# Kernel tuning notes

Measured on AMD Instinct MI355X. Metric: run time of the kernel, lower is better.

Reference implementation:

```python
import jax, jax.numpy as jnp
from jax import lax
import numpy as np

B, N, E, F = 32, 256, 8, 16
NEIGH = 31            # neighbourhood_size
K1 = NEIGH + 1        # subgraph size = neigh_size + 1


def setup_inputs() -> dict:
    rng = np.random.default_rng(0)
    # Connected symmetric adjacency: backbone chain + random extra pairs (no self loops).
    A = np.zeros((B, N, N), np.float32)
    i = np.arange(N - 1)
    A[:, i, i + 1] = 1.0
    A[:, i + 1, i] = 1.0
    for b in range(B):
        pairs = rng.integers(0, N, size=(N, 2))
        pairs = pairs[pairs[:, 0] != pairs[:, 1]]
        A[b, pairs[:, 0], pairs[:, 1]] = 1.0
        A[b, pairs[:, 1], pairs[:, 0]] = 1.0
    A[:, np.arange(N), np.arange(N)] = 0.0
    key = jax.random.key(0)
    k1, k2 = jax.random.split(key)
    edges = jax.random.normal(k1, (B, N, N, E), dtype=jnp.float32)
    feats = jax.random.normal(k2, (B, N, F), dtype=jnp.float32)
    return {"adj_batch": jnp.asarray(A), "edges_batch": edges, "features_batch": feats}


def _bfs(adj_bool, start):
    """Ordered BFS from `start`, collecting K1 vertices (matches get_neighbours:
    FIFO queue, neighbours enqueued in ascending index order, dedup vs seen)."""
    n = adj_bool.shape[0]
    queue = jnp.zeros((n + 1,), jnp.int32).at[0].set(start)  # slot n is a dummy sink
    seen = jnp.zeros((n,), bool).at[start].set(True)
    processed = jnp.zeros((K1,), jnp.int32)

    def body(i, st):
        queue, seen, head, tail, processed = st
        cur = queue[head]
        processed = processed.at[i].set(cur)
        nbr = adj_bool[cur] & ~seen                      # new frontier, index order
        cum = jnp.cumsum(nbr.astype(jnp.int32))
        pos = jnp.where(nbr, tail + cum - 1, n)          # compacted queue slots
        queue = queue.at[pos].set(jnp.arange(n, dtype=jnp.int32))
        return queue, seen | nbr, head + 1, tail + cum[-1], processed

    st = lax.fori_loop(0, K1, body, (queue, seen, jnp.int32(0), jnp.int32(1), processed))
    return st[4]  # [K1] BFS ordering


def reference(adj_batch, edges_batch, features_batch):
    adj_bool = adj_batch != 0
    starts = jnp.arange(adj_batch.shape[1], dtype=jnp.int32)
    # proc: [B, N, K1] local->original vertex mapping per (graph, centre vertex)
    proc = jax.vmap(lambda ab: jax.vmap(lambda s: _bfs(ab, s))(starts))(adj_bool)

    def gather(adj, edges, feats, p):
        pi = p[:, :, None]                               # [N, K1, 1]
        pj = p[:, None, :]                               # [N, 1, K1]
        sub_adj = adj[pi, pj]                            # [N, K1, K1]
        mask = (sub_adj != 0)[..., None]
        sub_edges = jnp.where(mask, edges[pi, pj], 0.0)  # [N, K1, K1, E]
        sub_feats = feats[p]                             # [N, K1, F]
        return sub_adj, sub_edges, sub_feats

    return jax.vmap(gather)(adj_batch, edges_batch, features_batch, proc)
```

## Files before the change

### kernel.cpp

```cpp
#include <hip/hip_runtime.h>
#include <stdint.h>

#define Bb 32
#define Nn 256
#define Ee 8
#define Ff 16
#define K1 32

typedef unsigned long long u64;
typedef float f32x4 __attribute__((ext_vector_type(4)));

__global__ void bitmask_kernel(const float* __restrict__ adj, u64* __restrict__ bm) {
    int wave = (blockIdx.x << 2) + (threadIdx.x >> 6);
    int lane = threadIdx.x & 63;
    const float* row = adj + (size_t)wave * Nn;
#pragma unroll
    for (int w = 0; w < 4; ++w) {
        float v = row[w * 64 + lane];
        u64 m = __ballot(v != 0.0f);
        if (lane == 0) bm[(size_t)wave * 4 + w] = m;
    }
}

__global__ void bfs_kernel(const u64* __restrict__ bm, uint32_t* __restrict__ proc32) {
    __shared__ u64 bml[Nn * 4];
    __shared__ uint8_t order[64 * K1];
    int b = blockIdx.x >> 2;
    int g = blockIdx.x & 3;
    int t = threadIdx.x;
#pragma unroll
    for (int k = 0; k < 16; ++k) bml[t + k * 64] = bm[(size_t)b * 1024 + t + k * 64];
    __syncthreads();

    int s = g * 64 + t;
    u64 seen[4];
#pragma unroll
    for (int w = 0; w < 4; ++w) seen[w] = (w == (s >> 6)) ? (1ull << (s & 63)) : 0ull;
    order[t * K1] = (uint8_t)s;
    int count = 1;
    for (int i = 0; i < count && count < K1; ++i) {
        int cur = order[t * K1 + i];
#pragma unroll
        for (int w = 0; w < 4; ++w) {
            u64 nw = bml[cur * 4 + w] & ~seen[w];
            seen[w] |= nw;
            while (nw) {
                int bit = __builtin_ctzll(nw);
                nw &= nw - 1;
                if (count < K1) order[t * K1 + count++] = (uint8_t)(w * 64 + bit);
                else break;
            }
        }
    }
    __syncthreads();
    const uint32_t* ord32 = (const uint32_t*)order;
#pragma unroll
    for (int k = 0; k < 8; ++k)
        proc32[(size_t)b * 2048 + g * 512 + t + k * 64] = ord32[t + k * 64];
}

__global__ void gather_kernel(const f32x4* __restrict__ e4,
                              const f32x4* __restrict__ feats4,
                              const u64* __restrict__ bm,
                              const uint32_t* __restrict__ proc32,
                              float* __restrict__ out) {
    int bs = blockIdx.x;
    int b = bs >> 8;
    int t = threadIdx.x;
    __shared__ int p[K1];
    __shared__ u64 bmrow[K1][4];

    if (t < 8) {
        uint32_t w = proc32[(size_t)bs * 8 + t];
        p[t * 4 + 0] = w & 255;
        p[t * 4 + 1] = (w >> 8) & 255;
        p[t * 4 + 2] = (w >> 16) & 255;
        p[t * 4 + 3] = (w >> 24) & 255;
    }
    __syncthreads();
    if (t < 128) {
        int i = t >> 2, w = t & 3;
        bmrow[i][w] = bm[((size_t)b * 256 + p[i]) * 4 + w];
    }
    __syncthreads();

    f32x4* out0 = (f32x4*)(out) + (size_t)bs * 256;
    {
        int i = t >> 3;
        int j0 = (t & 7) * 4;
        f32x4 a;
        int pj;
        pj = p[j0 + 0]; a.x = (float)((bmrow[i][pj >> 6] >> (pj & 63)) & 1ull);
        pj = p[j0 + 1]; a.y = (float)((bmrow[i][pj >> 6] >> (pj & 63)) & 1ull);
        pj = p[j0 + 2]; a.z = (float)((bmrow[i][pj >> 6] >> (pj & 63)) & 1ull);
        pj = p[j0 + 3]; a.w = (float)((bmrow[i][pj >> 6] >> (pj & 63)) & 1ull);
        __builtin_nontemporal_store(a, out0 + t);
    }

    f32x4* out2 = (f32x4*)(out + 75497472ull) + (size_t)bs * 128;
    if (t < 128) {
        int i = t >> 2, f4 = t & 3;
        f32x4 v = feats4[((size_t)b * 256 + p[i]) * 4 + f4];
        __builtin_nontemporal_store(v, out2 + t);
    }

    f32x4* out1 = (f32x4*)(out + 8388608ull) + (size_t)bs * 2048;
#pragma unroll
    for (int k = 0; k < 8; ++k) {
        int v = t + k * 256;
        int i = v >> 6, j = (v >> 1) & 31, h = v & 1;
        int pi = p[i], pj = p[j];
        bool m = (bmrow[i][pj >> 6] >> (pj & 63)) & 1ull;
        f32x4 val = (f32x4){0.f, 0.f, 0.f, 0.f};
        if (m) val = e4[(((size_t)b * 256 + pi) * 256 + pj) * 2 + h];
        __builtin_nontemporal_store(val, out1 + v);
    }
}

extern "C" void kernel_launch(void* const* d_in, const int* in_sizes, int n_in,
                              void* d_out, int out_size, void* d_ws, size_t ws_size,
                              hipStream_t stream) {
    const float* adj   = (const float*)d_in[0];
    const float* edges = (const float*)d_in[1];
    const float* feats = (const float*)d_in[2];
    float* out = (float*)d_out;

    u64* bm = (u64*)d_ws;
    uint32_t* proc32 = (uint32_t*)((char*)d_ws + (size_t)Bb * Nn * 4 * sizeof(u64));

    bitmask_kernel<<<Bb * Nn / 4, 256, 0, stream>>>(adj, bm);
    bfs_kernel<<<Bb * 4, 64, 0, stream>>>(bm, proc32);
    gather_kernel<<<Bb * Nn, 256, 0, stream>>>((const f32x4*)edges, (const f32x4*)feats,
                                               bm, proc32, out);
}
```

Measured before the change: 91.89 us.

## Fuse BFS into gather kernel, one serial BFS per block

Merges the BFS kernel into the gather kernel. Each block now loads its graph's 8KB bitmask into shared memory, and thread 0 runs the BFS for that block's start vertex serially before the gather. This removes one kernel launch and the proc buffer round trip through global memory, but every block now stalls on a single-thread serial BFS and redundantly reloads the graph bitmask. Nontemporal stores are also replaced with plain stores.

Measured after the change: 158.0 us. 72.0% more time.

```diff
diff --git a/kernel.cpp b/kernel.cpp
--- a/kernel.cpp
+++ b/kernel.cpp
@@ -22,86 +22,65 @@
     }
 }
 
-__global__ void bfs_kernel(const u64* __restrict__ bm, uint32_t* __restrict__ proc32) {
+__global__ void fused_kernel(const f32x4* __restrict__ e4,
+                             const f32x4* __restrict__ feats4,
+                             const u64* __restrict__ bm,
+                             float* __restrict__ out) {
+    int bs = blockIdx.x;
+    int b = bs >> 8;
+    int s = bs & 255;
+    int t = threadIdx.x;
     __shared__ u64 bml[Nn * 4];
-    __shared__ uint8_t order[64 * K1];
-    int b = blockIdx.x >> 2;
-    int g = blockIdx.x & 3;
-    int t = threadIdx.x;
+    __shared__ int p[K1];
+
 #pragma unroll
-    for (int k = 0; k < 16; ++k) bml[t + k * 64] = bm[(size_t)b * 1024 + t + k * 64];
+    for (int k = 0; k < 4; ++k) bml[t + k * 256] = bm[(size_t)b * 1024 + t + k * 256];
     __syncthreads();
 
-    int s = g * 64 + t;
-    u64 seen[4];
+    if (t == 0) {
+        u64 seen[4];
 #pragma unroll
-    for (int w = 0; w < 4; ++w) seen[w] = (w == (s >> 6)) ? (1ull << (s & 63)) : 0ull;
-    order[t * K1] = (uint8_t)s;
-    int count = 1;
-    for (int i = 0; i < count && count < K1; ++i) {
-        int cur = order[t * K1 + i];
+        for (int w = 0; w < 4; ++w) seen[w] = (w == (s >> 6)) ? (1ull << (s & 63)) : 0ull;
+        uint8_t order[K1];
+        order[0] = (uint8_t)s;
+        int count = 1;
+        for (int i = 0; i < count && count < K1; ++i) {
+            int cur = order[i];
 #pragma unroll
-        for (int w = 0; w < 4; ++w) {
-            u64 nw = bml[cur * 4 + w] & ~seen[w];
-            seen[w] |= nw;
-            while (nw) {
-                int bit = __builtin_ctzll(nw);
-                nw &= nw - 1;
-                if (count < K1) order[t * K1 + count++] = (uint8_t)(w * 64 + bit);
-                else break;
+            for (int w = 0; w < 4; ++w) {
+                u64 nw = bml[cur * 4 + w] & ~seen[w];
+                seen[w] |= nw;
+                while (nw) {
+                    int bit = __builtin_ctzll(nw);
+                    nw &= nw - 1;
+                    if (count < K1) order[count++] = (uint8_t)(w * 64 + bit);
+                    else break;
+                }
             }
         }
-    }
-    __syncthreads();
-    const uint32_t* ord32 = (const uint32_t*)order;
 #pragma unroll
-    for (int k = 0; k < 8; ++k)
-        proc32[(size_t)b * 2048 + g * 512 + t + k * 64] = ord32[t + k * 64];
-}
-
-__global__ void gather_kernel(const f32x4* __restrict__ e4,
-                              const f32x4* __restrict__ feats4,
-                              const u64* __restrict__ bm,
-                              const uint32_t* __restrict__ proc32,
-                              float* __restrict__ out) {
-    int bs = blockIdx.x;
-    int b = bs >> 8;
-    int t = threadIdx.x;
-    __shared__ int p[K1];
-    __shared__ u64 bmrow[K1][4];
-
-    if (t < 8) {
-        uint32_t w = proc32[(size_t)bs * 8 + t];
-        p[t * 4 + 0] = w & 255;
-        p[t * 4 + 1] = (w >> 8) & 255;
-        p[t * 4 + 2] = (w >> 16) & 255;
-        p[t * 4 + 3] = (w >> 24) & 255;
-    }
-    __syncthreads();
-    if (t < 128) {
-        int i = t >> 2, w = t & 3;
-        bmrow[i][w] = bm[((size_t)b * 256 + p[i]) * 4 + w];
+        for (int i = 0; i < K1; ++i) p[i] = order[i];
     }
     __syncthreads();
 
     f32x4* out0 = (f32x4*)(out) + (size_t)bs * 256;
     {
         int i = t >> 3;
+        int pi4 = p[i] * 4;
         int j0 = (t & 7) * 4;
         f32x4 a;
         int pj;
-        pj = p[j0 + 0]; a.x = (float)((bmrow[i][pj >> 6] >> (pj & 63)) & 1ull);
-        pj = p[j0 + 1]; a.y = (float)((bmrow[i][pj >> 6] >> (pj & 63)) & 1ull);
-        pj = p[j0 + 2]; a.z = (float)((bmrow[i][pj >> 6] >> (pj & 63)) & 1ull);
-        pj = p[j0 + 3]; a.w = (float)((bmrow[i][pj >> 6] >> (pj & 63)) & 1ull);
-        __builtin_nontemporal_store(a, out0 + t);
+        pj = p[j0 + 0]; a.x = (float)((bml[pi4 + (pj >> 6)] >> (pj & 63)) & 1ull);
+        pj = p[j0 + 1]; a.y = (float)((bml[pi4 + (pj >> 6)] >> (pj & 63)) & 1ull);
+        pj = p[j0 + 2]; a.z = (float)((bml[pi4 + (pj >> 6)] >> (pj & 63)) & 1ull);
+        pj = p[j0 + 3]; a.w = (float)((bml[pi4 + (pj >> 6)] >> (pj & 63)) & 1ull);
+        out0[t] = a;
     }
 
     f32x4* out2 = (f32x4*)(out + 75497472ull) + (size_t)bs * 128;
     if (t < 128) {
         int i = t >> 2, f4 = t & 3;
-        f32x4 v = feats4[((size_t)b * 256 + p[i]) * 4 + f4];
-        __builtin_nontemporal_store(v, out2 + t);
+        out2[t] = feats4[((size_t)b * 256 + p[i]) * 4 + f4];
     }
 
     f32x4* out1 = (f32x4*)(out + 8388608ull) + (size_t)bs * 2048;
@@ -110,10 +89,10 @@
         int v = t + k * 256;
         int i = v >> 6, j = (v >> 1) & 31, h = v & 1;
         int pi = p[i], pj = p[j];
-        bool m = (bmrow[i][pj >> 6] >> (pj & 63)) & 1ull;
+        bool m = (bml[pi * 4 + (pj >> 6)] >> (pj & 63)) & 1ull;
         f32x4 val = (f32x4){0.f, 0.f, 0.f, 0.f};
         if (m) val = e4[(((size_t)b * 256 + pi) * 256 + pj) * 2 + h];
-        __builtin_nontemporal_store(val, out1 + v);
+        out1[v] = val;
     }
 }
 
@@ -126,10 +105,8 @@
     float* out = (float*)d_out;
 
     u64* bm = (u64*)d_ws;
-    uint32_t* proc32 = (uint32_t*)((char*)d_ws + (size_t)Bb * Nn * 4 * sizeof(u64));
 
     bitmask_kernel<<<Bb * Nn / 4, 256, 0, stream>>>(adj, bm);
-    bfs_kernel<<<Bb * 4, 64, 0, stream>>>(bm, proc32);
-    gather_kernel<<<Bb * Nn, 256, 0, stream>>>((const f32x4*)edges, (const f32x4*)feats,
-                                               bm, proc32, out);
+    fused_kernel<<<Bb * Nn, 256, 0, stream>>>((const f32x4*)edges, (const f32x4*)feats,
+                                              bm, out);
 }
```
